# Kernel tuning notes

Measured on AMD Instinct MI355X. Metric: run time of the kernel, lower is better.

## Reference

```python
import jax, jax.numpy as jnp
import numpy as np

B, S = 1024, 64          # batch, num clips (att_size)
R = 1024                 # CG_rnn_size
E = 1024                 # CG_input_encoding_size
CD = 1024                # clip_context_dim
ED = 1024                # event_context_dim
H = 512                  # CG_att_hid_size


def setup_inputs() -> dict:
    key = jax.random.key(0)
    ks = jax.random.split(key, 20)
    s = 0.02
    return {
        "xt": jax.random.normal(ks[0], (B, E), jnp.float32),
        "video": jax.random.normal(ks[1], (B, 1024), jnp.float32),
        "event": jax.random.normal(ks[2], (B, ED), jnp.float32),
        "clip": jax.random.normal(ks[3], (B, S, CD), jnp.float32),
        "clip_mask": jax.random.randint(ks[4], (B, S), 0, 2, jnp.int32),
        "state_h": jax.random.normal(ks[5], (2, B, R), jnp.float32),
        "state_c": jax.random.normal(ks[6], (2, B, R), jnp.float32),
        # LSTMCell 0 (input = event ++ xt -> ED+E)
        "W_ih0": jax.random.normal(ks[7], (4 * R, ED + E), jnp.float32) * s,
        "b_ih0": jnp.zeros((4 * R,), jnp.float32),
        "W_hh0": jax.random.normal(ks[8], (4 * R, R), jnp.float32) * s,
        "b_hh0": jnp.zeros((4 * R,), jnp.float32),
        # LSTMCell 1 (input = att ++ xt -> CD+E)
        "W_ih1": jax.random.normal(ks[9], (4 * R, CD + E), jnp.float32) * s,
        "b_ih1": jnp.zeros((4 * R,), jnp.float32),
        "W_hh1": jax.random.normal(ks[10], (4 * R, R), jnp.float32) * s,
        "b_hh1": jnp.zeros((4 * R,), jnp.float32),
        # Attention params
        "W_ctx": jax.random.normal(ks[11], (H, CD), jnp.float32) * s,
        "b_ctx": jnp.zeros((H,), jnp.float32),
        "W_h2a": jax.random.normal(ks[12], (H, R), jnp.float32) * s,
        "b_h2a": jnp.zeros((H,), jnp.float32),
        "W_alpha": jax.random.normal(ks[13], (1, H), jnp.float32) * s,
        "b_alpha": jnp.zeros((1,), jnp.float32),
    }


def _lstm_cell(x, h, c, W_ih, b_ih, W_hh, b_hh):
    gates = x @ W_ih.T + b_ih + h @ W_hh.T + b_hh  # [B, 4R]
    i, f, g, o = jnp.split(gates, 4, axis=-1)
    i, f, o = jax.nn.sigmoid(i), jax.nn.sigmoid(f), jax.nn.sigmoid(o)
    g = jnp.tanh(g)
    c_new = f * c + i * g
    h_new = o * jnp.tanh(c_new)
    return h_new, c_new


def _attention(h, att_feats, att_mask, W_ctx, b_ctx, W_h2a, b_h2a, W_alpha, b_alpha):
    att = att_feats @ W_ctx.T + b_ctx                 # [B, S, H]
    att_h = h @ W_h2a.T + b_h2a                       # [B, H]
    dot = jnp.tanh(att + att_h[:, None, :])           # [B, S, H]
    scores = (dot @ W_alpha.T + b_alpha)[..., 0]      # [B, S]
    weight = jax.nn.softmax(scores, axis=1)
    m = att_mask.astype(weight.dtype)
    weight = weight * m
    weight = weight / jnp.sum(weight, axis=1, keepdims=True)
    return jnp.einsum('bs,bsd->bd', weight, att_feats)  # [B, CD]


def reference(xt, video, event, clip, clip_mask, state_h, state_c,
              W_ih0, b_ih0, W_hh0, b_hh0, W_ih1, b_ih1, W_hh1, b_hh1,
              W_ctx, b_ctx, W_h2a, b_h2a, W_alpha, b_alpha):
    pre_h1 = state_h[1]
    # stream 0: torch.cat((xt, event), 1)
    h0, c0 = _lstm_cell(jnp.concatenate([xt, event], axis=1),
                        state_h[0], state_c[0], W_ih0, b_ih0, W_hh0, b_hh0)
    att = _attention(pre_h1, clip, clip_mask,
                     W_ctx, b_ctx, W_h2a, b_h2a, W_alpha, b_alpha)
    h1, c1 = _lstm_cell(jnp.concatenate([xt, att], axis=1),
                        state_h[1], state_c[1], W_ih1, b_ih1, W_hh1, b_hh1)
    # dropout layers are identity in eval mode
    output = jnp.concatenate([h0, h1], axis=1)        # [B, 2R]
    new_h = jnp.stack([h0, h1])
    new_c = jnp.stack([c0, c1])
    return output, new_h, new_c
```

## Files before the change

### kernel.cpp

```cpp
#include <hip/hip_runtime.h>

typedef short short8 __attribute__((ext_vector_type(8)));
typedef short sshort4 __attribute__((ext_vector_type(4)));
typedef float floatx4 __attribute__((ext_vector_type(4)));
typedef unsigned short u16;

__device__ __forceinline__ u16 cvt_bf(float x) {
  unsigned u = __float_as_uint(x);
  unsigned r = 0x7FFFu + ((u >> 16) & 1u);
  return (u16)((u + r) >> 16);
}
__device__ __forceinline__ float bf2f(u16 h) {
  return __uint_as_float(((unsigned)h) << 16);
}
__device__ __forceinline__ void gll16(const u16* g, u16* l) {
  __builtin_amdgcn_global_load_lds(
      (__attribute__((address_space(1))) void*)(void*)const_cast<u16*>(g),
      (__attribute__((address_space(3))) void*)(void*)l, 16, 0, 0);
}
__device__ __forceinline__ short8 load_cvt8(const float* g) {
  const float4 v0 = *(const float4*)g;
  const float4 v1 = *(const float4*)(g + 4);
  short8 p;
  p[0] = (short)cvt_bf(v0.x); p[1] = (short)cvt_bf(v0.y);
  p[2] = (short)cvt_bf(v0.z); p[3] = (short)cvt_bf(v0.w);
  p[4] = (short)cvt_bf(v1.x); p[5] = (short)cvt_bf(v1.y);
  p[6] = (short)cvt_bf(v1.z); p[7] = (short)cvt_bf(v1.w);
  return p;
}
__device__ __forceinline__ float fast_tanh(float x) {
  float t = __expf(-2.f * fabsf(x));
  float r = 1.f - 2.f * t / (1.f + t);
  return copysignf(r, x);
}
__device__ __forceinline__ float fast_sigm(float x) {
  return 1.f / (1.f + __expf(-x));
}

#define MAXSEG 13
struct ConvArgs {
  const float* src[MAXSEG];
  u16* dst[MAXSEG];
  unsigned lw[MAXSEG];
  unsigned dstride[MAXSEG];
  unsigned blk0[MAXSEG + 1];
  int nseg;
};
__device__ __forceinline__ void conv_seg_body(const ConvArgs& a, unsigned blk) {
  int s = 0;
  for (int i = 1; i < a.nseg; ++i) if (blk >= a.blk0[i]) s = i;
  const unsigned e0 = (blk - a.blk0[s]) * 2048u + threadIdx.x * 8u;
  short8 p = {};
  u16* d;
  const float* src = a.src[s];
  if (src) {
    p = load_cvt8(src + e0);
    const unsigned row = e0 >> a.lw[s];
    const unsigned col = e0 & ((1u << a.lw[s]) - 1u);
    d = a.dst[s] + (size_t)row * a.dstride[s] + col;
  } else {
    d = a.dst[s] + e0;
  }
  *(short8*)d = p;
}
__global__ __launch_bounds__(256)
void convert_seg(ConvArgs a) { conv_seg_body(a, blockIdx.x); }

__global__ __launch_bounds__(256)
void conv_flat(const float* __restrict__ src, u16* __restrict__ dst) {
  const size_t e = (size_t)blockIdx.x * 2048 + threadIdx.x * 8;
  *(short8*)(dst + e) = load_cvt8(src + e);
}
__global__ __launch_bounds__(256)
void zerof(float* __restrict__ p) { p[blockIdx.x * 256 + threadIdx.x] = 0.f; }

template<int AF32, int BF32>
__device__ __forceinline__ void gemm_body_t(
    const void* __restrict__ Av, int sa, const void* __restrict__ Bv, int sb,
    int K, int Mbase, int Nbase, u16* sA, u16* sB, floatx4 (&acc)[4][4])
{
  const int tid = threadIdx.x, lane = tid & 63, w = tid >> 6;
  const int quad = lane >> 4, l15 = lane & 15;
  const int wm = w >> 1, wn = w & 1;
  const int srow = lane >> 3;
  const int sslot = (lane & 7) ^ srow;

  for (int k0 = 0; k0 < K; k0 += 64) {
    __syncthreads();
#pragma unroll
    for (int j = 0; j < 4; ++j) {
      const int c = w + 4 * j;
      const int row = c * 8 + srow;
      if (AF32) {
        const float* g = (const float*)Av + (size_t)(Mbase + row) * sa + k0 + sslot * 8;
        *(short8*)&sA[c * 512 + lane * 8] = load_cvt8(g);
      } else {
        gll16((const u16*)Av + (size_t)(Mbase + row) * sa + k0 + sslot * 8, &sA[c * 512]);
      }
      if (BF32) {
        const float* g = (const float*)Bv + (size_t)(Nbase + row) * sb + k0 + sslot * 8;
        *(short8*)&sB[c * 512 + lane * 8] = load_cvt8(g);
      } else {
        gll16((const u16*)Bv + (size_t)(Nbase + row) * sb + k0 + sslot * 8, &sB[c * 512]);
      }
    }
    __syncthreads();
#pragma unroll
    for (int ks = 0; ks < 2; ++ks) {
      short8 af[4], bf[4];
#pragma unroll
      for (int mt = 0; mt < 4; ++mt) {
        const int row = wm * 64 + mt * 16 + l15;
        af[mt] = *(const short8*)&sA[row * 64 + ((ks * 4 + quad) ^ (row & 7)) * 8];
      }
#pragma unroll
      for (int nt = 0; nt < 4; ++nt) {
        const int row = wn * 64 + nt * 16 + l15;
        bf[nt] = *(const short8*)&sB[row * 64 + ((ks * 4 + quad) ^ (row & 7)) * 8];
      }
#pragma unroll
      for (int mt = 0; mt < 4; ++mt)
#pragma unroll
        for (int nt = 0; nt < 4; ++nt)
          acc[mt][nt] = __builtin_amdgcn_mfma_f32_16x16x32_bf16(af[mt], bf[nt], acc[mt][nt], 0, 0, 0);
    }
  }
}

__device__ __forceinline__ void epi_store(
    floatx4 (&acc)[4][4], const float* __restrict__ bias0,
    const float* __restrict__ bias1, float* __restrict__ out,
    int N, int Mbase, int Nbase)
{
  const int tid = threadIdx.x, lane = tid & 63, w = tid >> 6;
  const int quad = lane >> 4, l15 = lane & 15;
  const int wm = w >> 1, wn = w & 1;
#pragma unroll
  for (int nt = 0; nt < 4; ++nt) {
    const int col = Nbase + wn * 64 + nt * 16 + l15;
    const float bc = bias0 ? (bias0[col] + bias1[col]) : 0.f;
#pragma unroll
    for (int mt = 0; mt < 4; ++mt) {
      const int rb = Mbase + wm * 64 + mt * 16 + quad * 4;
#pragma unroll
      for (int r = 0; r < 4; ++r)
        out[(size_t)(rb + r) * N + col] = acc[mt][nt][r] + bc;
    }
  }
}

__device__ __forceinline__ void epi_score(
    floatx4 (&acc)[4][4], const float* __restrict__ atth,
    const float* __restrict__ Walpha, float* __restrict__ scores,
    int Mbase, int Nbase)
{
  const int tid = threadIdx.x, lane = tid & 63, w = tid >> 6;
  const int quad = lane >> 4, l15 = lane & 15;
  const int wm = w >> 1, wn = w & 1;
  const int b = (Mbase + wm * 64) >> 6;
  float rs[4][4] = {};
#pragma unroll
  for (int nt = 0; nt < 4; ++nt) {
    const int col = Nbase + wn * 64 + nt * 16 + l15;
    const float wa = Walpha[col];
    const float ah = atth[(size_t)b * 512 + col];
#pragma unroll
    for (int mt = 0; mt < 4; ++mt)
#pragma unroll
      for (int r = 0; r < 4; ++r)
        rs[mt][r] += wa * fast_tanh(acc[mt][nt][r] + ah);
  }
#pragma unroll
  for (int mt = 0; mt < 4; ++mt)
#pragma unroll
    for (int r = 0; r < 4; ++r) {
      float v = rs[mt][r];
      v += __shfl_xor(v, 1); v += __shfl_xor(v, 2);
      v += __shfl_xor(v, 4); v += __shfl_xor(v, 8);
      if (l15 == 0)
        atomicAdd(&scores[Mbase + wm * 64 + mt * 16 + quad * 4 + r], v);
    }
}

__device__ __forceinline__ void lstm_body(
    const float* __restrict__ gates, const float* __restrict__ g1b,
    const float* __restrict__ cprev, float* __restrict__ out, int st, int blk)
{
  const int idx = blk * 256 + (int)threadIdx.x;
  const int b = idx >> 8;
  const int r4 = (idx & 255) * 4;
  const float* g = gates + (size_t)b * 4096 + r4;
  float4 gi = *(const float4*)g;
  float4 gf = *(const float4*)(g + 1024);
  float4 gg = *(const float4*)(g + 2048);
  float4 go = *(const float4*)(g + 3072);
  if (g1b) {
    const float* h = g1b + (size_t)b * 4096 + r4;
    const float4 hi = *(const float4*)h;
    const float4 hf = *(const float4*)(h + 1024);
    const float4 hg = *(const float4*)(h + 2048);
    const float4 ho = *(const float4*)(h + 3072);
    gi.x += hi.x; gi.y += hi.y; gi.z += hi.z; gi.w += hi.w;
    gf.x += hf.x; gf.y += hf.y; gf.z += hf.z; gf.w += hf.w;
    gg.x += hg.x; gg.y += hg.y; gg.z += hg.z; gg.w += hg.w;
    go.x += ho.x; go.y += ho.y; go.z += ho.z; go.w += ho.w;
  }
  const float4 c = *(const float4*)(cprev + (size_t)b * 1024 + r4);
  float4 cn, hn;
  cn.x = fast_sigm(gf.x) * c.x + fast_sigm(gi.x) * fast_tanh(gg.x);  hn.x = fast_sigm(go.x) * fast_tanh(cn.x);
  cn.y = fast_sigm(gf.y) * c.y + fast_sigm(gi.y) * fast_tanh(gg.y);  hn.y = fast_sigm(go.y) * fast_tanh(cn.y);
  cn.z = fast_sigm(gf.z) * c.z + fast_sigm(gi.z) * fast_tanh(gg.z);  hn.z = fast_sigm(go.z) * fast_tanh(cn.z);
  cn.w = fast_sigm(gf.w) * c.w + fast_sigm(gi.w) * fast_tanh(gg.w);  hn.w = fast_sigm(go.w) * fast_tanh(cn.w);
  *(float4*)(out + (size_t)b * 2048 + st * 1024 + r4) = hn;
  *(float4*)(out + 2097152 + (size_t)st * 1048576 + (size_t)b * 1024 + r4) = hn;
  *(float4*)(out + 4194304 + (size_t)st * 1048576 + (size_t)b * 1024 + r4) = cn;
}

template<int MODE>
__global__ __launch_bounds__(256, 3)
void gemm128(const u16* __restrict__ A, int sa, const u16* __restrict__ B, int sb,
             const float* __restrict__ bias0, const float* __restrict__ bias1,
             float* __restrict__ out, int N, int K,
             const float* __restrict__ atth, const float* __restrict__ Walpha,
             float* __restrict__ scores, int row0,
             const u16* A2, const u16* B2,
             const float* bias0b, const float* bias1b, float* out2)
{
  if (blockIdx.z) { A = A2; B = B2; bias0 = bias0b; bias1 = bias1b; out = out2; }
  __shared__ u16 sA[128 * 64];
  __shared__ u16 sB[128 * 64];
  const int Mbase = blockIdx.y * 128, Nbase = blockIdx.x * 128;
  floatx4 acc[4][4] = {};
  gemm_body_t<0, 0>(A, sa, B, sb, K, Mbase, Nbase, sA, sB, acc);
  if (MODE == 0) epi_store(acc, bias0, bias1, out, N, Mbase, Nbase);
  else           epi_score(acc, atth, Walpha, scores, row0 + Mbase, Nbase);
}

__global__ __launch_bounds__(256)
void softmax_k(const float* __restrict__ scores, const int* __restrict__ mask,
               float* __restrict__ wbuf)
{
  const int b = blockIdx.x * 4 + (threadIdx.x >> 6);
  const int s = threadIdx.x & 63;
  const float v = scores[b * 64 + s];
  float mx = v;
#pragma unroll
  for (int d = 32; d; d >>= 1) mx = fmaxf(mx, __shfl_xor(mx, d));
  const float e = __expf(v - mx) * (float)mask[b * 64 + s];
  float den = e;
#pragma unroll
  for (int d = 32; d; d >>= 1) den += __shfl_xor(den, d);
  wbuf[b * 64 + s] = e / den;
}

template<int BF>
__global__ __launch_bounds__(128)
void ctx_att(const float* __restrict__ clipf, const u16* __restrict__ clipb,
             const float* __restrict__ wbuf, u16* __restrict__ A1)
{
  __shared__ float w[64];
  const int b = blockIdx.x, tid = threadIdx.x;
  if (tid < 64) w[tid] = wbuf[b * 64 + tid];
  __syncthreads();
  const int c8 = tid * 8;
  float a[8] = {};
  if (BF) {
    const u16* base = clipb + (size_t)b * 65536 + c8;
#pragma unroll 4
    for (int s = 0; s < 64; ++s) {
      const float wt = w[s];
      const short8 c = *(const short8*)(base + (size_t)s * 1024);
#pragma unroll
      for (int j = 0; j < 8; ++j) a[j] += wt * bf2f((u16)c[j]);
    }
  } else {
    const float* base = clipf + (size_t)b * 65536 + c8;
#pragma unroll 4
    for (int s = 0; s < 64; ++s) {
      const float wt = w[s];
      const float4 v0 = *(const float4*)(base + (size_t)s * 1024);
      const float4 v1 = *(const float4*)(base + (size_t)s * 1024 + 4);
      a[0] += wt * v0.x; a[1] += wt * v0.y; a[2] += wt * v0.z; a[3] += wt * v0.w;
      a[4] += wt * v1.x; a[5] += wt * v1.y; a[6] += wt * v1.z; a[7] += wt * v1.w;
    }
  }
  short8 p;
#pragma unroll
  for (int j = 0; j < 8; ++j) p[j] = (short)cvt_bf(a[j]);
  *(short8*)&A1[(size_t)b * 3072 + 1024 + c8] = p;
}

__global__ __launch_bounds__(256)
void lstm_ew(const float* __restrict__ gates, const float* __restrict__ cprev,
             float* __restrict__ out, int st)
{
  lstm_body(gates, nullptr, cprev, out, st, blockIdx.x);
}

__global__ __launch_bounds__(256)
void atth_conv(ConvArgs a, const float* __restrict__ h1p,
               const float* __restrict__ Wh2a, const float* __restrict__ b_h2a,
               const float* __restrict__ b_ctx, float* __restrict__ atth)
{
  __shared__ u16 sA[128 * 64];
  __shared__ u16 sB[128 * 64];
  const int bid = blockIdx.x;
  if (bid < 32) {
    const int Nbase = (bid & 3) * 128, Mbase = (bid >> 2) * 128;
    floatx4 acc[4][4] = {};
    gemm_body_t<1, 1>(h1p, 1024, Wh2a, 1024, 1024, Mbase, Nbase, sA, sB, acc);
    epi_store(acc, b_h2a, b_ctx, atth, 512, Mbase, Nbase);
    return;
  }
  conv_seg_body(a, bid - 32);
}

__global__ __launch_bounds__(256, 3)
void g0score(const u16* __restrict__ A0, const u16* __restrict__ W0,
             const float* __restrict__ bi0, const float* __restrict__ bh0,
             float* __restrict__ gates0,
             const float* __restrict__ clip, const u16* __restrict__ Wc,
             const float* __restrict__ atth, const float* __restrict__ Walpha,
             float* __restrict__ scores)
{
  __shared__ u16 sA[128 * 64];
  __shared__ u16 sB[128 * 64];
  floatx4 acc[4][4] = {};
  const int bid = blockIdx.x;
  if (bid < 256) {
    const int Nbase = (bid & 31) * 128, Mbase = (bid >> 5) * 128;
    gemm_body_t<0, 0>(A0, 3072, W0, 3072, 3072, Mbase, Nbase, sA, sB, acc);
    epi_store(acc, bi0, bh0, gates0, 4096, Mbase, Nbase);
  } else {
    const int t = bid - 256;
    const int Nbase = (t & 3) * 128, Mbase = (t >> 2) * 128;
    gemm_body_t<1, 0>(clip, 1024, Wc, 1024, 1024, Mbase, Nbase, sA, sB, acc);
    epi_score(acc, atth, Walpha, scores, Mbase, Nbase);
  }
}

__global__ __launch_bounds__(256)
void sm_ctx(const float* __restrict__ scores, const int* __restrict__ cmask,
            const float* __restrict__ clip, u16* __restrict__ A1)
{
  __shared__ float w[64];
  const int b = blockIdx.x, tid = threadIdx.x;
  if (tid < 64) {
    const float v = scores[b * 64 + tid];
    float mx = v;
#pragma unroll
    for (int d = 32; d; d >>= 1) mx = fmaxf(mx, __shfl_xor(mx, d));
    const float e = __expf(v - mx) * (float)cmask[b * 64 + tid];
    float den = e;
#pragma unroll
    for (int d = 32; d; d >>= 1) den += __shfl_xor(den, d);
    w[tid] = e / den;
  }
  __syncthreads();
  const int c4 = tid * 4;
  float a0 = 0.f, a1 = 0.f, a2 = 0.f, a3 = 0.f;
  const float* base = clip + (size_t)b * 65536 + c4;
#pragma unroll 4
  for (int s = 0; s < 64; ++s) {
    const float wt = w[s];
    const float4 v = *(const float4*)(base + (size_t)s * 1024);
    a0 += wt * v.x; a1 += wt * v.y; a2 += wt * v.z; a3 += wt * v.w;
  }
  sshort4 p;
  p[0] = (short)cvt_bf(a0); p[1] = (short)cvt_bf(a1);
  p[2] = (short)cvt_bf(a2); p[3] = (short)cvt_bf(a3);
  *(sshort4*)&A1[(size_t)b * 3072 + 1024 + c4] = p;
}

__global__ __launch_bounds__(256, 3)
void g1ew(const u16* __restrict__ A1, const u16* __restrict__ W1,
          const float* __restrict__ bi1, const float* __restrict__ bh1,
          float* __restrict__ g1a, float* __restrict__ g1b,
          const float* __restrict__ gates0, const float* __restrict__ c0p,
          float* __restrict__ out)
{
  __shared__ u16 sA[128 * 64];
  __shared__ u16 sB[128 * 64];
  const int bid = blockIdx.x;
  if (bid < 512) {
    floatx4 acc[4][4] = {};
    const int half = bid >> 8;
    const int t = bid & 255;
    const int Nbase = (t & 31) * 128, Mbase = (t >> 5) * 128;
    const int k0 = half * 1536;
    gemm_body_t<0, 0>(A1 + k0, 3072, W1 + k0, 3072, 1536, Mbase, Nbase, sA, sB, acc);
    if (half == 0) epi_store(acc, bi1, bh1, g1a, 4096, Mbase, Nbase);
    else           epi_store(acc, nullptr, nullptr, g1b, 4096, Mbase, Nbase);
  } else {
    lstm_body(gates0, nullptr, c0p, out, 0, bid - 512);
  }
}

__global__ __launch_bounds__(256)
void ew1sum(const float* __restrict__ g1a, const float* __restrict__ g1b,
            const float* __restrict__ c1p, float* __restrict__ out)
{
  lstm_body(g1a, g1b, c1p, out, 1, blockIdx.x);
}

extern "C" void kernel_launch(void* const* d_in, const int* in_sizes, int n_in,
                              void* d_out, int out_size, void* d_ws, size_t ws_size,
                              hipStream_t stream) {
  (void)in_sizes; (void)n_in; (void)out_size;
  const float* xt      = (const float*)d_in[0];
  const float* event   = (const float*)d_in[2];
  const float* clip    = (const float*)d_in[3];
  const int*   cmask   = (const int*)d_in[4];
  const float* state_h = (const float*)d_in[5];
  const float* state_c = (const float*)d_in[6];
  const float* W_ih0   = (const float*)d_in[7];
  const float* b_ih0   = (const float*)d_in[8];
  const float* W_hh0   = (const float*)d_in[9];
  const float* b_hh0   = (const float*)d_in[10];
  const float* W_ih1   = (const float*)d_in[11];
  const float* b_ih1   = (const float*)d_in[12];
  const float* W_hh1   = (const float*)d_in[13];
  const float* b_hh1   = (const float*)d_in[14];
  const float* W_ctx   = (const float*)d_in[15];
  const float* b_ctx   = (const float*)d_in[16];
  const float* W_h2a   = (const float*)d_in[17];
  const float* b_h2a   = (const float*)d_in[18];
  const float* W_alpha = (const float*)d_in[19];

  const float* h0p = state_h;
  const float* h1p = state_h + 1048576;
  const float* c0p = state_c;
  const float* c1p = state_c + 1048576;
  float* out = (float*)d_out;

  if (ws_size >= 116654080) {
    char* p = (char*)d_ws;
    float* gates0 = (float*)p; p += 16777216;
    float* g1a    = (float*)p; p += 16777216;
    float* g1b    = (float*)p; p += 16777216;
    u16* A0 = (u16*)p; p += 6291456;
    u16* A1 = (u16*)p; p += 6291456;
    u16* W0 = (u16*)p; p += 25165824;
    u16* W1 = (u16*)p; p += 25165824;
    u16* Wc = (u16*)p; p += 1048576;
    float* atth   = (float*)p; p += 2097152;
    float* scores = (float*)p;

    ConvArgs ca{};
    {
      const float* srcs[11] = {W_ctx, W_ih0, W_hh0, W_ih1, W_hh1,
                               xt, event, h0p, xt, h1p, nullptr};
      u16* dsts[11] = {Wc, W0, W0 + 2048, W1, W1 + 2048,
                       A0, A0 + 1024, A0 + 2048, A1, A1 + 2048, (u16*)scores};
      const unsigned lws[11]  = {10, 11, 10, 11, 10, 10, 10, 10, 10, 10, 17};
      const unsigned dstr[11] = {1024, 3072, 3072, 3072, 3072,
                                 3072, 3072, 3072, 3072, 3072, 0};
      const unsigned nblk[11] = {256, 4096, 2048, 4096, 2048,
                                 512, 512, 512, 512, 512, 64};
      unsigned acc = 0;
      for (int i = 0; i < 11; ++i) {
        ca.src[i] = srcs[i]; ca.dst[i] = dsts[i];
        ca.lw[i] = lws[i]; ca.dstride[i] = dstr[i];
        ca.blk0[i] = acc; acc += nblk[i];
      }
      ca.blk0[11] = acc; ca.nseg = 11;
      atth_conv<<<32 + acc, 256, 0, stream>>>(ca, h1p, W_h2a, b_h2a, b_ctx, atth);
    }

    g0score<<<2304, 256, 0, stream>>>(A0, W0, b_ih0, b_hh0, gates0,
                                      clip, Wc, atth, W_alpha, scores);

    sm_ctx<<<1024, 256, 0, stream>>>(scores, cmask, clip, A1);

    g1ew<<<1536, 256, 0, stream>>>(A1, W1, b_ih1, b_hh1, g1a, g1b,
                                   gates0, c0p, out);

    ew1sum<<<1024, 256, 0, stream>>>(g1a, g1b, c1p, out);
    return;
  }

  int NC; bool grouped;
  if      (ws_size >= 207618048) { NC = 1; grouped = true;  }
  else if (ws_size >= 106954752) { NC = 4; grouped = true;  }
  else                           { NC = 8; grouped = false; }

  char* p = (char*)d_ws;
  float* gates0 = (float*)p; p += 16777216;
  float* gates1 = gates0;
  if (grouped) { gates1 = (float*)p; p += 16777216; }
  u16* A0 = (u16*)p; p += 6291456;
  u16* A1 = (u16*)p; p += 6291456;
  u16* W0 = (u16*)p; p += 25165824;
  u16* Wc = (u16*)p; p += 1048576;
  u16* Wh = (u16*)p; p += 1048576;
  u16* clipb = (u16*)p;
  u16* W1 = (u16*)p;
  float* atth   = gates0;
  float* wbuf   = gates0 + 524288;
  float* scores = gates0 + 589824;

  ConvArgs ca{};
  {
    const float* srcs[9] = {W_ctx, W_h2a, W_ih0, W_hh0, xt, event, h0p, xt, h1p};
    u16* dsts[9] = {Wc, Wh, W0, W0 + 2048, A0, A0 + 1024, A0 + 2048, A1, A1 + 2048};
    const unsigned lws[9]  = {10, 10, 11, 10, 10, 10, 10, 10, 10};
    const unsigned dstr[9] = {1024, 1024, 3072, 3072, 3072, 3072, 3072, 3072, 3072};
    const unsigned nblk[9] = {256, 256, 4096, 2048, 512, 512, 512, 512, 512};
    unsigned acc = 0;
    for (int i = 0; i < 9; ++i) {
      ca.src[i] = srcs[i]; ca.dst[i] = dsts[i];
      ca.lw[i] = lws[i]; ca.dstride[i] = dstr[i];
      ca.blk0[i] = acc; acc += nblk[i];
    }
    ca.blk0[9] = acc; ca.nseg = 9;
    convert_seg<<<acc, 256, 0, stream>>>(ca);
  }

  zerof<<<256, 256, 0, stream>>>(scores);

  gemm128<0><<<dim3(4, 8, 1), 256, 0, stream>>>(
      A1 + 2048, 3072, Wh, 1024, b_h2a, b_ctx, atth, 512, 1024,
      nullptr, nullptr, nullptr, 0, nullptr, nullptr, nullptr, nullptr, nullptr);

  const int rows = 65536 / NC;
  for (int c = 0; c < NC; ++c) {
    conv_flat<<<rows * 1024 / 2048, 256, 0, stream>>>(clip + (size_t)c * rows * 1024, clipb);
    gemm128<1><<<dim3(4, rows / 128, 1), 256, 0, stream>>>(
        clipb, 1024, Wc, 1024, nullptr, nullptr, nullptr, 512, 1024,
        atth, W_alpha, scores, c * rows,
        nullptr, nullptr, nullptr, nullptr, nullptr);
  }

  softmax_k<<<256, 256, 0, stream>>>(scores, cmask, wbuf);

  if (NC == 1) ctx_att<1><<<1024, 128, 0, stream>>>(clip, clipb, wbuf, A1);
  else         ctx_att<0><<<1024, 128, 0, stream>>>(clip, clipb, wbuf, A1);

  ConvArgs cb{};
  {
    const float* srcs[2] = {W_ih1, W_hh1};
    u16* dsts[2] = {W1, W1 + 2048};
    const unsigned lws[2] = {11, 10};
    const unsigned nblk[2] = {4096, 2048};
    unsigned acc = 0;
    for (int i = 0; i < 2; ++i) {
      cb.src[i] = srcs[i]; cb.dst[i] = dsts[i];
      cb.lw[i] = lws[i]; cb.dstride[i] = 3072;
      cb.blk0[i] = acc; acc += nblk[i];
    }
    cb.blk0[2] = acc; cb.nseg = 2;
    convert_seg<<<acc, 256, 0, stream>>>(cb);
  }

  if (grouped) {
    gemm128<0><<<dim3(32, 8, 2), 256, 0, stream>>>(
        A0, 3072, W0, 3072, b_ih0, b_hh0, gates0, 4096, 3072,
        nullptr, nullptr, nullptr, 0,
        A1, W1, b_ih1, b_hh1, gates1);
    lstm_ew<<<1024, 256, 0, stream>>>(gates0, c0p, out, 0);
    lstm_ew<<<1024, 256, 0, stream>>>(gates1, c1p, out, 1);
  } else {
    gemm128<0><<<dim3(32, 8, 1), 256, 0, stream>>>(
        A0, 3072, W0, 3072, b_ih0, b_hh0, gates0, 4096, 3072,
        nullptr, nullptr, nullptr, 0, nullptr, nullptr, nullptr, nullptr, nullptr);
    lstm_ew<<<1024, 256, 0, stream>>>(gates0, c0p, out, 0);
    gemm128<0><<<dim3(32, 8, 1), 256, 0, stream>>>(
        A1, 3072, W1, 3072, b_ih1, b_hh1, gates0, 4096, 3072,
        nullptr, nullptr, nullptr, 0, nullptr, nullptr, nullptr, nullptr, nullptr);
    lstm_ew<<<1024, 256, 0, stream>>>(gates0, c1p, out, 1);
  }
}
```

Before: 707.5 us.

## Pre-convert clip to bf16 and hoist xt/h1 GEMM part before attention

Clip features are converted to bf16 once in the conversion kernel and reused by both the score GEMM and the softmax-context reduction, halving those reads. The xt and h1 portions of the LSTM1 gate GEMM now run alongside the LSTM0 and score GEMMs, so only the attention-context K-slice remains after softmax. The LSTM0 elementwise step moves into the softmax kernel. This needs a much larger workspace (an extra 128MB buffer); if the workspace is too small the code falls back to the old path. Writing the full bf16 clip copy costs extra traffic up front.

```diff
diff --git a/kernel.cpp b/kernel.cpp
--- a/kernel.cpp
+++ b/kernel.cpp
@@ -316,12 +316,15 @@
 }
 
 __global__ __launch_bounds__(256, 3)
-void g0score(const u16* __restrict__ A0, const u16* __restrict__ W0,
-             const float* __restrict__ bi0, const float* __restrict__ bh0,
-             float* __restrict__ gates0,
-             const float* __restrict__ clip, const u16* __restrict__ Wc,
-             const float* __restrict__ atth, const float* __restrict__ Walpha,
-             float* __restrict__ scores)
+void g0g1score(const u16* __restrict__ A0, const u16* __restrict__ W0,
+               const float* __restrict__ bi0, const float* __restrict__ bh0,
+               float* __restrict__ gates0,
+               const u16* __restrict__ A1, const u16* __restrict__ W1,
+               const float* __restrict__ bi1, const float* __restrict__ bh1,
+               float* __restrict__ g1a,
+               const u16* __restrict__ clipb, const u16* __restrict__ Wc,
+               const float* __restrict__ atth, const float* __restrict__ Walpha,
+               float* __restrict__ scores)
 {
   __shared__ u16 sA[128 * 64];
   __shared__ u16 sB[128 * 64];
@@ -331,20 +334,30 @@
     const int Nbase = (bid & 31) * 128, Mbase = (bid >> 5) * 128;
     gemm_body_t<0, 0>(A0, 3072, W0, 3072, 3072, Mbase, Nbase, sA, sB, acc);
     epi_store(acc, bi0, bh0, gates0, 4096, Mbase, Nbase);
+  } else if (bid < 512) {
+    const int t = bid - 256;
+    const int Nbase = (t & 31) * 128, Mbase = (t >> 5) * 128;
+    gemm_body_t<0, 0>(A1, 3072, W1, 3072, 1024, Mbase, Nbase, sA, sB, acc);
+    gemm_body_t<0, 0>(A1 + 2048, 3072, W1 + 2048, 3072, 1024, Mbase, Nbase, sA, sB, acc);
+    epi_store(acc, bi1, bh1, g1a, 4096, Mbase, Nbase);
   } else {
-    const int t = bid - 256;
+    const int t = bid - 512;
     const int Nbase = (t & 3) * 128, Mbase = (t >> 2) * 128;
-    gemm_body_t<1, 0>(clip, 1024, Wc, 1024, 1024, Mbase, Nbase, sA, sB, acc);
+    gemm_body_t<0, 0>(clipb, 1024, Wc, 1024, 1024, Mbase, Nbase, sA, sB, acc);
     epi_score(acc, atth, Walpha, scores, Mbase, Nbase);
   }
 }
 
 __global__ __launch_bounds__(256)
-void sm_ctx(const float* __restrict__ scores, const int* __restrict__ cmask,
-            const float* __restrict__ clip, u16* __restrict__ A1)
-{
+void smctx_ew0(const float* __restrict__ scores, const int* __restrict__ cmask,
+               const u16* __restrict__ clipb, u16* __restrict__ A1,
+               const float* __restrict__ gates0, const float* __restrict__ c0p,
+               float* __restrict__ out)
+{
+  const int bid = blockIdx.x, tid = threadIdx.x;
+  if (bid >= 1024) { lstm_body(gates0, nullptr, c0p, out, 0, bid - 1024); return; }
   __shared__ float w[64];
-  const int b = blockIdx.x, tid = threadIdx.x;
+  const int b = bid;
   if (tid < 64) {
     const float v = scores[b * 64 + tid];
     float mx = v;
@@ -359,12 +372,13 @@
   __syncthreads();
   const int c4 = tid * 4;
   float a0 = 0.f, a1 = 0.f, a2 = 0.f, a3 = 0.f;
-  const float* base = clip + (size_t)b * 65536 + c4;
+  const u16* base = clipb + (size_t)b * 65536 + c4;
 #pragma unroll 4
   for (int s = 0; s < 64; ++s) {
     const float wt = w[s];
-    const float4 v = *(const float4*)(base + (size_t)s * 1024);
-    a0 += wt * v.x; a1 += wt * v.y; a2 += wt * v.z; a3 += wt * v.w;
+    const sshort4 v = *(const sshort4*)(base + (size_t)s * 1024);
+    a0 += wt * bf2f((u16)v[0]); a1 += wt * bf2f((u16)v[1]);
+    a2 += wt * bf2f((u16)v[2]); a3 += wt * bf2f((u16)v[3]);
   }
   sshort4 p;
   p[0] = (short)cvt_bf(a0); p[1] = (short)cvt_bf(a1);
@@ -373,27 +387,16 @@
 }
 
 __global__ __launch_bounds__(256, 3)
-void g1ew(const u16* __restrict__ A1, const u16* __restrict__ W1,
-          const float* __restrict__ bi1, const float* __restrict__ bh1,
-          float* __restrict__ g1a, float* __restrict__ g1b,
-          const float* __restrict__ gates0, const float* __restrict__ c0p,
-          float* __restrict__ out)
+void g1att(const u16* __restrict__ A1, const u16* __restrict__ W1,
+           float* __restrict__ g1b)
 {
   __shared__ u16 sA[128 * 64];
   __shared__ u16 sB[128 * 64];
-  const int bid = blockIdx.x;
-  if (bid < 512) {
-    floatx4 acc[4][4] = {};
-    const int half = bid >> 8;
-    const int t = bid & 255;
-    const int Nbase = (t & 31) * 128, Mbase = (t >> 5) * 128;
-    const int k0 = half * 1536;
-    gemm_body_t<0, 0>(A1 + k0, 3072, W1 + k0, 3072, 1536, Mbase, Nbase, sA, sB, acc);
-    if (half == 0) epi_store(acc, bi1, bh1, g1a, 4096, Mbase, Nbase);
-    else           epi_store(acc, nullptr, nullptr, g1b, 4096, Mbase, Nbase);
-  } else {
-    lstm_body(gates0, nullptr, c0p, out, 0, bid - 512);
-  }
+  floatx4 acc[4][4] = {};
+  const int t = blockIdx.x;
+  const int Nbase = (t & 31) * 128, Mbase = (t >> 5) * 128;
+  gemm_body_t<0, 0>(A1 + 1024, 3072, W1 + 1024, 3072, 1024, Mbase, Nbase, sA, sB, acc);
+  epi_store(acc, nullptr, nullptr, g1b, 4096, Mbase, Nbase);
 }
 
 __global__ __launch_bounds__(256)
@@ -433,7 +436,7 @@
   const float* c1p = state_c + 1048576;
   float* out = (float*)d_out;
 
-  if (ws_size >= 116654080) {
+  if (ws_size >= 250871808) {
     char* p = (char*)d_ws;
     float* gates0 = (float*)p; p += 16777216;
     float* g1a    = (float*)p; p += 16777216;
@@ -443,37 +446,39 @@
     u16* W0 = (u16*)p; p += 25165824;
     u16* W1 = (u16*)p; p += 25165824;
     u16* Wc = (u16*)p; p += 1048576;
+    u16* clipb = (u16*)p; p += 134217728;
     float* atth   = (float*)p; p += 2097152;
     float* scores = (float*)p;
 
     ConvArgs ca{};
     {
-      const float* srcs[11] = {W_ctx, W_ih0, W_hh0, W_ih1, W_hh1,
+      const float* srcs[12] = {clip, W_ih0, W_hh0, W_ih1, W_hh1, W_ctx,
                                xt, event, h0p, xt, h1p, nullptr};
-      u16* dsts[11] = {Wc, W0, W0 + 2048, W1, W1 + 2048,
+      u16* dsts[12] = {clipb, W0, W0 + 2048, W1, W1 + 2048, Wc,
                        A0, A0 + 1024, A0 + 2048, A1, A1 + 2048, (u16*)scores};
-      const unsigned lws[11]  = {10, 11, 10, 11, 10, 10, 10, 10, 10, 10, 17};
-      const unsigned dstr[11] = {1024, 3072, 3072, 3072, 3072,
+      const unsigned lws[12]  = {10, 11, 10, 11, 10, 10, 10, 10, 10, 10, 10, 17};
+      const unsigned dstr[12] = {1024, 3072, 3072, 3072, 3072, 1024,
                                  3072, 3072, 3072, 3072, 3072, 0};
-      const unsigned nblk[11] = {256, 4096, 2048, 4096, 2048,
+      const unsigned nblk[12] = {32768, 4096, 2048, 4096, 2048, 256,
                                  512, 512, 512, 512, 512, 64};
       unsigned acc = 0;
-      for (int i = 0; i < 11; ++i) {
+      for (int i = 0; i < 12; ++i) {
         ca.src[i] = srcs[i]; ca.dst[i] = dsts[i];
         ca.lw[i] = lws[i]; ca.dstride[i] = dstr[i];
         ca.blk0[i] = acc; acc += nblk[i];
       }
-      ca.blk0[11] = acc; ca.nseg = 11;
+      ca.blk0[12] = acc; ca.nseg = 12;
       atth_conv<<<32 + acc, 256, 0, stream>>>(ca, h1p, W_h2a, b_h2a, b_ctx, atth);
     }
 
-    g0score<<<2304, 256, 0, stream>>>(A0, W0, b_ih0, b_hh0, gates0,
-                                      clip, Wc, atth, W_alpha, scores);
-
-    sm_ctx<<<1024, 256, 0, stream>>>(scores, cmask, clip, A1);
-
-    g1ew<<<1536, 256, 0, stream>>>(A1, W1, b_ih1, b_hh1, g1a, g1b,
-                                   gates0, c0p, out);
+    g0g1score<<<2560, 256, 0, stream>>>(A0, W0, b_ih0, b_hh0, gates0,
+                                        A1, W1, b_ih1, b_hh1, g1a,
+                                        clipb, Wc, atth, W_alpha, scores);
+
+    smctx_ew0<<<2048, 256, 0, stream>>>(scores, cmask, clipb, A1,
+                                        gates0, c0p, out);
+
+    g1att<<<256, 256, 0, stream>>>(A1, W1, g1b);
 
     ew1sum<<<1024, 256, 0, stream>>>(g1a, g1b, c1p, out);
     return;
```

Measured after the change: 706.6 us. About the same (-0.1%).
